# Kernel tuning notes

Measured on AMD Instinct MI355X. Metric: run time of the kernel, lower is better.

## Reference

```python
import jax, jax.numpy as jnp
import numpy as np

HIDDEN_DIM = 512
N = 2 * HIDDEN_DIM  # 1024
B, T_K = 32, 2048


def setup_inputs() -> dict:
    key = jax.random.key(0)
    ks = jax.random.split(key, 10)
    s_t_hat = jax.random.normal(ks[0], (B, N), dtype=jnp.float32)
    encoder_outputs = jax.random.normal(ks[1], (B, T_K, N), dtype=jnp.float32)
    encoder_feature = jax.random.normal(ks[2], (B * T_K, N), dtype=jnp.float32)
    stmt_feature = jax.random.uniform(ks[3], (B, T_K), dtype=jnp.float32) * 0.01
    enc_padding_mask = jnp.ones((B, T_K), dtype=jnp.float32)
    coverage = jax.random.uniform(ks[4], (B, T_K), dtype=jnp.float32)
    # learned params
    W_dec = jax.random.normal(ks[5], (N, N), dtype=jnp.float32) / np.sqrt(N)
    b_dec = jnp.zeros((N,), dtype=jnp.float32)
    v_w = jax.random.normal(ks[6], (N,), dtype=jnp.float32) / np.sqrt(N)
    W_c = jax.random.normal(ks[7], (N,), dtype=jnp.float32)  # Linear(1, N, bias=False)
    return {
        "s_t_hat": s_t_hat,
        "encoder_outputs": encoder_outputs,
        "encoder_feature": encoder_feature,
        "stmt_feature": stmt_feature,
        "enc_padding_mask": enc_padding_mask,
        "coverage": coverage,
        "W_dec": W_dec,
        "b_dec": b_dec,
        "v_w": v_w,
        "W_c": W_c,
    }


def reference(s_t_hat, encoder_outputs, encoder_feature, stmt_feature,
              enc_padding_mask, coverage, W_dec, b_dec, v_w, W_c):
    b, t_k, n = encoder_outputs.shape
    # decode_proj: [b, n]
    dec_fea = s_t_hat @ W_dec.T + b_dec
    # broadcast-add decoder feature + coverage feature (Linear(1, n) == outer product)
    att_features = (encoder_feature.reshape(b, t_k, n)
                    + dec_fea[:, None, :]
                    + coverage[:, :, None] * W_c)  # [b, t_k, n]
    e = jnp.tanh(att_features)
    scores = jnp.einsum('btn,n->bt', e, v_w)  # v: Linear(n, 1, bias=False)
    attn_dist_ = jax.nn.softmax(scores, axis=1) * enc_padding_mask
    attn_dist = attn_dist_ / attn_dist_.sum(axis=1, keepdims=True)
    attn_dist = attn_dist + stmt_feature * enc_padding_mask
    c_t = jnp.einsum('bt,btn->bn', attn_dist, encoder_outputs)  # bmm
    coverage_out = coverage + attn_dist
    return (c_t, attn_dist, coverage_out)
```

## Files before the change

### kernel.cpp

```cpp
#include <hip/hip_runtime.h>

#define B   32
#define TK  2048
#define N   1024
#define NF4 256

#define OUT_CT   0
#define OUT_ATTN (B * N)
#define OUT_COV  (B * N + B * TK)

__device__ __forceinline__ float hw_exp2(float x) {
    return __builtin_amdgcn_exp2f(x);
}

__device__ __forceinline__ float fast_tanh(float x) {
    float t = hw_exp2(x * 2.8853900817779268f);
    return 1.0f - 2.0f * __builtin_amdgcn_rcpf(t + 1.0f);
}

__device__ __forceinline__ float wave_reduce_sum(float v) {
#pragma unroll
    for (int off = 32; off > 0; off >>= 1) v += __shfl_xor(v, off, 64);
    return v;
}

__global__ __launch_bounds__(256) void decfea_kernel(
    const float4* __restrict__ S,
    const float4* __restrict__ W,
    const float*  __restrict__ bias,
    float*        __restrict__ dec)
{
    int w    = blockIdx.x * 4 + (threadIdx.x >> 6);
    int lane = threadIdx.x & 63;
    int n    = w >> 3;
    int b0   = (w & 7) * 4;

    float4 wr[4];
#pragma unroll
    for (int j = 0; j < 4; ++j) wr[j] = W[n * NF4 + j * 64 + lane];

#pragma unroll
    for (int i = 0; i < 4; ++i) {
        int b = b0 + i;
        float acc = 0.0f;
#pragma unroll
        for (int j = 0; j < 4; ++j) {
            float4 s4 = S[b * NF4 + j * 64 + lane];
            acc += s4.x * wr[j].x + s4.y * wr[j].y + s4.z * wr[j].z + s4.w * wr[j].w;
        }
        acc = wave_reduce_sum(acc);
        if (lane == 0) dec[b * N + n] = acc + bias[n];
    }
}

__global__ __launch_bounds__(256) void scores_kernel(
    const float4* __restrict__ EF,
    const float4* __restrict__ DEC,
    const float4* __restrict__ WC,
    const float4* __restrict__ VW,
    const float*  __restrict__ cov,
    float*        __restrict__ scores)
{
    int r    = blockIdx.x * 4 + (threadIdx.x >> 6);
    int lane = threadIdx.x & 63;
    int b    = r >> 11;
    float c  = cov[r];

    const float4* ef = EF + (size_t)r * NF4;
    const float4* de = DEC + b * NF4;

    float partial = 0.0f;
#pragma unroll
    for (int j = 0; j < 4; ++j) {
        int f = j * 64 + lane;
        float4 e  = ef[f];
        float4 d  = de[f];
        float4 wc = WC[f];
        float4 vw = VW[f];
        partial += fast_tanh(e.x + d.x + c * wc.x) * vw.x;
        partial += fast_tanh(e.y + d.y + c * wc.y) * vw.y;
        partial += fast_tanh(e.z + d.z + c * wc.z) * vw.z;
        partial += fast_tanh(e.w + d.w + c * wc.w) * vw.w;
    }
    partial = wave_reduce_sum(partial);
    if (lane == 0) scores[r] = partial;
}

__global__ __launch_bounds__(256) void softmax_kernel(
    const float* __restrict__ scores,
    const float* __restrict__ mask,
    const float* __restrict__ stmt,
    const float* __restrict__ coverage,
    float*       __restrict__ attn_ws,
    float*       __restrict__ out)
{
    int b = blockIdx.x, tid = threadIdx.x;
    __shared__ float red[256];

    float s[8];
    float m = -1e30f;
#pragma unroll
    for (int k = 0; k < 8; ++k) {
        s[k] = scores[b * TK + k * 256 + tid];
        m = fmaxf(m, s[k]);
    }
    red[tid] = m;
    __syncthreads();
    for (int step = 128; step > 0; step >>= 1) {
        if (tid < step) red[tid] = fmaxf(red[tid], red[tid + step]);
        __syncthreads();
    }
    float M = red[0];
    __syncthreads();

    float e[8];
    float loc = 0.0f;
#pragma unroll
    for (int k = 0; k < 8; ++k) {
        int t = k * 256 + tid;
        e[k] = hw_exp2((s[k] - M) * 1.4426950408889634f) * mask[b * TK + t];
        loc += e[k];
    }
    red[tid] = loc;
    __syncthreads();
    for (int step = 128; step > 0; step >>= 1) {
        if (tid < step) red[tid] += red[tid + step];
        __syncthreads();
    }
    float inv = 1.0f / red[0];

#pragma unroll
    for (int k = 0; k < 8; ++k) {
        int t = k * 256 + tid;
        int r = b * TK + t;
        float a = e[k] * inv + stmt[r] * mask[r];
        attn_ws[r] = a;
        out[OUT_ATTN + r] = a;
        out[OUT_COV + r] = coverage[r] + a;
    }

    float4 z = {0.0f, 0.0f, 0.0f, 0.0f};
    ((float4*)(out + OUT_CT))[b * NF4 + tid] = z;
}

__global__ __launch_bounds__(256) void ct_kernel(
    const float4* __restrict__ EO,
    const float*  __restrict__ attn,
    float*        __restrict__ ct)
{
    int s = blockIdx.x;
    int b = blockIdx.y;
    int tid = threadIdx.x;

    __shared__ float wbuf[128];
    if (tid < 128) wbuf[tid] = attn[b * TK + s * 128 + tid];
    __syncthreads();

    float4 acc = {0.0f, 0.0f, 0.0f, 0.0f};
    const float4* eo = EO + ((size_t)b * TK + s * 128) * NF4 + tid;
#pragma unroll 4
    for (int tt = 0; tt < 128; ++tt) {
        float w  = wbuf[tt];
        float4 v = eo[(size_t)tt * NF4];
        acc.x += w * v.x;
        acc.y += w * v.y;
        acc.z += w * v.z;
        acc.w += w * v.w;
    }
    float* dst = ct + b * N + tid * 4;
    atomicAdd(dst + 0, acc.x);
    atomicAdd(dst + 1, acc.y);
    atomicAdd(dst + 2, acc.z);
    atomicAdd(dst + 3, acc.w);
}

extern "C" void kernel_launch(void* const* d_in, const int* in_sizes, int n_in,
                              void* d_out, int out_size, void* d_ws, size_t ws_size,
                              hipStream_t stream) {
    const float* s_t_hat = (const float*)d_in[0];
    const float* EO      = (const float*)d_in[1];
    const float* EF      = (const float*)d_in[2];
    const float* stmt    = (const float*)d_in[3];
    const float* mask    = (const float*)d_in[4];
    const float* cov     = (const float*)d_in[5];
    const float* Wdec    = (const float*)d_in[6];
    const float* bdec    = (const float*)d_in[7];
    const float* vw      = (const float*)d_in[8];
    const float* wc      = (const float*)d_in[9];

    float* out = (float*)d_out;
    float* ws  = (float*)d_ws;
    float* dec    = ws;
    float* scores = ws + B * N;
    float* attn   = ws + B * N + B * TK;

    decfea_kernel<<<2048, 256, 0, stream>>>(
        (const float4*)s_t_hat, (const float4*)Wdec, bdec, dec);

    scores_kernel<<<16384, 256, 0, stream>>>(
        (const float4*)EF, (const float4*)dec, (const float4*)wc,
        (const float4*)vw, cov, scores);

    softmax_kernel<<<B, 256, 0, stream>>>(scores, mask, stmt, cov, attn, out);

    ct_kernel<<<dim3(16, B), 256, 0, stream>>>(
        (const float4*)EO, attn, out + OUT_CT);
}
```

Measured before the change: 523.7 us.

## Process 8 rows per wave in scores; replace ct atomics with slice partials plus reduce

The scores kernel now gives each wave 8 consecutive rows, loading W_c, v_w and the decoder feature into registers once per wave instead of once per row. The weighted context sum is split into 32 time slices per batch. Each slice writes a partial vector to workspace, and a separate reduce kernel sums them, replacing the zero-init plus float atomicAdd scheme. This doubles the number of blocks in the memory-bound context pass and removes atomics, at the cost of one extra launch and a small partial buffer round trip.

```diff
diff --git a/kernel.cpp b/kernel.cpp
--- a/kernel.cpp
+++ b/kernel.cpp
@@ -4,6 +4,7 @@
 #define TK  2048
 #define N   1024
 #define NF4 256
+#define NSLICE 32
 
 #define OUT_CT   0
 #define OUT_ATTN (B * N)
@@ -61,29 +62,37 @@
     const float*  __restrict__ cov,
     float*        __restrict__ scores)
 {
-    int r    = blockIdx.x * 4 + (threadIdx.x >> 6);
+    int wave = blockIdx.x * 4 + (threadIdx.x >> 6);
     int lane = threadIdx.x & 63;
-    int b    = r >> 11;
-    float c  = cov[r];
-
-    const float4* ef = EF + (size_t)r * NF4;
-    const float4* de = DEC + b * NF4;
-
-    float partial = 0.0f;
+    int r0   = wave * 8;
+    int b    = r0 >> 11;
+
+    float4 wc[4], vw[4], de[4];
 #pragma unroll
     for (int j = 0; j < 4; ++j) {
         int f = j * 64 + lane;
-        float4 e  = ef[f];
-        float4 d  = de[f];
-        float4 wc = WC[f];
-        float4 vw = VW[f];
-        partial += fast_tanh(e.x + d.x + c * wc.x) * vw.x;
-        partial += fast_tanh(e.y + d.y + c * wc.y) * vw.y;
-        partial += fast_tanh(e.z + d.z + c * wc.z) * vw.z;
-        partial += fast_tanh(e.w + d.w + c * wc.w) * vw.w;
-    }
-    partial = wave_reduce_sum(partial);
-    if (lane == 0) scores[r] = partial;
+        wc[j] = WC[f];
+        vw[j] = VW[f];
+        de[j] = DEC[b * NF4 + f];
+    }
+
+#pragma unroll
+    for (int k = 0; k < 8; ++k) {
+        int r   = r0 + k;
+        float c = cov[r];
+        const float4* ef = EF + (size_t)r * NF4;
+        float p = 0.0f;
+#pragma unroll
+        for (int j = 0; j < 4; ++j) {
+            float4 e = ef[j * 64 + lane];
+            p += fast_tanh(e.x + de[j].x + c * wc[j].x) * vw[j].x;
+            p += fast_tanh(e.y + de[j].y + c * wc[j].y) * vw[j].y;
+            p += fast_tanh(e.z + de[j].z + c * wc[j].z) * vw[j].z;
+            p += fast_tanh(e.w + de[j].w + c * wc[j].w) * vw[j].w;
+        }
+        p = wave_reduce_sum(p);
+        if (lane == 0) scores[r] = p;
+    }
 }
 
 __global__ __launch_bounds__(256) void softmax_kernel(
@@ -138,40 +147,47 @@
         out[OUT_ATTN + r] = a;
         out[OUT_COV + r] = coverage[r] + a;
     }
-
-    float4 z = {0.0f, 0.0f, 0.0f, 0.0f};
-    ((float4*)(out + OUT_CT))[b * NF4 + tid] = z;
-}
-
-__global__ __launch_bounds__(256) void ct_kernel(
+}
+
+__global__ __launch_bounds__(256) void ct_part_kernel(
     const float4* __restrict__ EO,
     const float*  __restrict__ attn,
-    float*        __restrict__ ct)
+    float4*       __restrict__ part)
 {
     int s = blockIdx.x;
     int b = blockIdx.y;
     int tid = threadIdx.x;
 
-    __shared__ float wbuf[128];
-    if (tid < 128) wbuf[tid] = attn[b * TK + s * 128 + tid];
+    __shared__ float wbuf[TK / NSLICE];
+    if (tid < TK / NSLICE) wbuf[tid] = attn[b * TK + s * (TK / NSLICE) + tid];
     __syncthreads();
 
     float4 acc = {0.0f, 0.0f, 0.0f, 0.0f};
-    const float4* eo = EO + ((size_t)b * TK + s * 128) * NF4 + tid;
-#pragma unroll 4
-    for (int tt = 0; tt < 128; ++tt) {
-        float w  = wbuf[tt];
-        float4 v = eo[(size_t)tt * NF4];
+    const float4* eo = EO + ((size_t)b * TK + s * (TK / NSLICE)) * NF4 + tid;
+#pragma unroll 8
+    for (int t = 0; t < TK / NSLICE; ++t) {
+        float w  = wbuf[t];
+        float4 v = eo[(size_t)t * NF4];
         acc.x += w * v.x;
         acc.y += w * v.y;
         acc.z += w * v.z;
         acc.w += w * v.w;
     }
-    float* dst = ct + b * N + tid * 4;
-    atomicAdd(dst + 0, acc.x);
-    atomicAdd(dst + 1, acc.y);
-    atomicAdd(dst + 2, acc.z);
-    atomicAdd(dst + 3, acc.w);
+    part[((size_t)s * B + b) * NF4 + tid] = acc;
+}
+
+__global__ __launch_bounds__(256) void ct_reduce_kernel(
+    const float4* __restrict__ part,
+    float4*       __restrict__ ct)
+{
+    int idx = blockIdx.x * 256 + threadIdx.x;
+    float4 a = {0.0f, 0.0f, 0.0f, 0.0f};
+#pragma unroll
+    for (int s = 0; s < NSLICE; ++s) {
+        float4 v = part[(size_t)s * (B * NF4) + idx];
+        a.x += v.x; a.y += v.y; a.z += v.z; a.w += v.w;
+    }
+    ct[idx] = a;
 }
 
 extern "C" void kernel_launch(void* const* d_in, const int* in_sizes, int n_in,
@@ -193,16 +209,20 @@
     float* dec    = ws;
     float* scores = ws + B * N;
     float* attn   = ws + B * N + B * TK;
+    float* part   = ws + B * N + 2 * B * TK;
 
     decfea_kernel<<<2048, 256, 0, stream>>>(
         (const float4*)s_t_hat, (const float4*)Wdec, bdec, dec);
 
-    scores_kernel<<<16384, 256, 0, stream>>>(
+    scores_kernel<<<2048, 256, 0, stream>>>(
         (const float4*)EF, (const float4*)dec, (const float4*)wc,
         (const float4*)vw, cov, scores);
 
     softmax_kernel<<<B, 256, 0, stream>>>(scores, mask, stmt, cov, attn, out);
 
-    ct_kernel<<<dim3(16, B), 256, 0, stream>>>(
-        (const float4*)EO, attn, out + OUT_CT);
-}
+    ct_part_kernel<<<dim3(NSLICE, B), 256, 0, stream>>>(
+        (const float4*)EO, attn, (float4*)part);
+
+    ct_reduce_kernel<<<B, 256, 0, stream>>>(
+        (const float4*)part, (float4*)(out + OUT_CT));
+}
```

Measured after the change: 532.0 us. About the same (+1.6%).
